# Performance work log

Measured on AMD Instinct MI355X. Metric: run time of the kernel, lower is better.

Reference implementation:

```python
import jax, jax.numpy as jnp
import numpy as np

B, L, P, C = 8, 4, 1024, 256
NH, NS = 8, 4
HD = C // NH  # 32
LEVEL_HW = [(64, 64), (32, 32), (16, 16), (8, 8)]


def setup_inputs() -> dict:
    key = jax.random.key(0)
    ks = jax.random.split(key, 14)
    inp = {
        "x": jax.random.normal(ks[0], (B, L, P, C), jnp.float32),
        # reference points are grid_sample coords in [-1, 1]
        "ref": jax.random.uniform(ks[1], (B, L, P, 2), jnp.float32, -0.9, 0.9),
    }
    for i, (h, w) in enumerate(LEVEL_HW):
        inp[f"feat{i}"] = jax.random.normal(ks[2 + i], (B, C, h, w), jnp.float32)
    inp["w_attn"] = jax.random.normal(ks[6], (C, NH * NS), jnp.float32) * 0.02
    inp["b_attn"] = jax.random.normal(ks[7], (NH * NS,), jnp.float32) * 0.02
    inp["w_off"] = jax.random.normal(ks[8], (C, 2 * NH * NS), jnp.float32) * 0.02
    inp["b_off"] = jax.random.normal(ks[9], (2 * NH * NS,), jnp.float32) * 0.02
    inp["embed_w"] = jax.random.normal(ks[10], (L, C, HD), jnp.float32) * 0.02
    inp["embed_b"] = jax.random.normal(ks[11], (L, HD), jnp.float32) * 0.02
    return inp


def grid_sample_bilinear(feat, grid):
    """torch.F.grid_sample(mode='bilinear', padding_mode='zeros', align_corners=True).
    feat: (B, C, H, W); grid: (B, Gh, Gw, 2) with (x, y) in [-1, 1].
    Returns (B, Gh, Gw, C)  (already permuted vs torch's (B, C, Gh, Gw))."""
    Bn, Cn, H, W = feat.shape
    fx = (grid[..., 0] + 1.0) * 0.5 * (W - 1)  # align_corners=True mapping
    fy = (grid[..., 1] + 1.0) * 0.5 * (H - 1)
    x0f = jnp.floor(fx)
    y0f = jnp.floor(fy)
    x0 = x0f.astype(jnp.int32)
    y0 = y0f.astype(jnp.int32)
    x1 = x0 + 1
    y1 = y0 + 1
    wx1 = fx - x0f
    wy1 = fy - y0f
    wx0 = 1.0 - wx1
    wy0 = 1.0 - wy1
    feat_hwc = jnp.transpose(feat, (0, 2, 3, 1))  # (B, H, W, C)

    def gather(yi, xi):
        valid = ((yi >= 0) & (yi < H) & (xi >= 0) & (xi < W)).astype(feat.dtype)
        yc = jnp.clip(yi, 0, H - 1)
        xc = jnp.clip(xi, 0, W - 1)
        v = jax.vmap(lambda f, y, x: f[y, x])(feat_hwc, yc, xc)  # (B, Gh, Gw, C)
        return v * valid[..., None]

    out = (gather(y0, x0) * (wy0 * wx0)[..., None]
           + gather(y0, x1) * (wy0 * wx1)[..., None]
           + gather(y1, x0) * (wy1 * wx0)[..., None]
           + gather(y1, x1) * (wy1 * wx1)[..., None])
    return out


def reference(x, ref, feat0, feat1, feat2, feat3,
              w_attn, b_attn, w_off, b_off, embed_w, embed_b):
    feats = [feat0, feat1, feat2, feat3]
    b, l, p, c = x.shape
    # attention weights: softmax over samples
    weights = jax.nn.softmax((x @ w_attn + b_attn).reshape(b, l, p, NH, NS), axis=-1)
    # sampling offsets, squashed by tanh
    offsets = jnp.tanh((x @ w_off + b_off).reshape(b, l, p, NH * NS, 2))
    pos = offsets + ref[:, :, :, None, :]  # (b, l, p, NH*NS, 2)
    sampled = []
    for i, f in enumerate(feats):
        s = grid_sample_bilinear(f, pos[:, i])  # (b, p, NH*NS, C_l)
        sampled.append(s @ embed_w[i] + embed_b[i])  # (b, p, NH*NS, HD)
    fs = jnp.stack(sampled, axis=1).reshape(b, l, p, NH, NS, HD)
    out = (weights[..., None] * fs).sum(axis=-2).reshape(b, l, p, NH * HD)
    return out
```

## Files before the change

### kernel.cpp

```cpp
#include <hip/hip_runtime.h>
#include <math.h>

#define B_   8
#define L_   4
#define P_   1024
#define C_   256
#define NH_  8
#define NS_  4
#define HD_  32

typedef _Float16 half8 __attribute__((ext_vector_type(8)));
typedef _Float16 half4 __attribute__((ext_vector_type(4)));
typedef float    f32x4 __attribute__((ext_vector_type(4)));

#define G_F     0u
#define SAMP_F  1392640u
#define WU_F    5586944u
#define ET_F    5611520u

__constant__ const int kGoff[4] = {0, 1048576, 1310720, 1376256};

#define XH2 72
#define LGS 100
#define FTS 40
#define NG_GPROJ 680

__global__ void k0_conv(const float* __restrict__ wa, const float* __restrict__ wo,
                        const float* __restrict__ embed_w,
                        _Float16* __restrict__ WuT, _Float16* __restrict__ ET16) {
  const int bx = blockIdx.x, t = threadIdx.x;
  if (bx < 96) {
    const int n = bx;
    const float v = (n < 32) ? wa[t * 32 + n] : wo[t * 64 + (n - 32)];
    WuT[n * 256 + t] = (_Float16)v;
  } else {
    const int i0 = (bx - 96) * 1024 + t * 4;
    const int l = i0 >> 13, rem = i0 & 8191;
    const int c = rem >> 5, e0 = rem & 31;
    const float4 v = *(const float4*)(embed_w + i0);
    _Float16* d = ET16 + l * 8192 + c;
    d[(e0 + 0) * 256] = (_Float16)v.x;
    d[(e0 + 1) * 256] = (_Float16)v.y;
    d[(e0 + 2) * 256] = (_Float16)v.z;
    d[(e0 + 3) * 256] = (_Float16)v.w;
  }
}

__global__ __launch_bounds__(256) void stage1(
    const float* __restrict__ f0, const float* __restrict__ f1,
    const float* __restrict__ f2, const float* __restrict__ f3,
    const _Float16* __restrict__ ET16, _Float16* __restrict__ g16,
    const float* __restrict__ x,
    const float* __restrict__ ref,
    const _Float16* __restrict__ WuT,
    const float* __restrict__ ba, const float* __restrict__ bo,
    float4* __restrict__ samp4)
{
  __shared__ float4 smraw4[1600];
  const int t = threadIdx.x;
  const int bx = blockIdx.x;
  const int lane = t & 63, wv = t >> 6;
  const int lr = lane & 15, kg = lane >> 4;

  if (bx < NG_GPROJ) {
    _Float16* flT = (_Float16*)smraw4;
    const int b = bx / 85;
    int sub = bx - b * 85, l, tile;
    const float* src;
    if (sub < 64)      { l = 0; tile = sub;      src = f0; }
    else if (sub < 80) { l = 1; tile = sub - 64; src = f1; }
    else if (sub < 84) { l = 2; tile = sub - 80; src = f2; }
    else               { l = 3; tile = 0;        src = f3; }
    const int Wl = 64 >> l, S = Wl * Wl;
    const int s0 = tile * 64;

    const float* sb = src + (size_t)b * C_ * S + s0;
    const _Float16* ETl = ET16 + (size_t)l * 8192;
    const int sl = t & 63, cb = (t >> 6) * 8;

    float vcur[8], vnext[8];
    #pragma unroll
    for (int i = 0; i < 8; ++i) vnext[i] = sb[(size_t)(cb + i) * S + sl];

    f32x4 acc0 = (f32x4){0.f, 0.f, 0.f, 0.f};
    f32x4 acc1 = (f32x4){0.f, 0.f, 0.f, 0.f};

    #pragma unroll
    for (int c = 0; c < 8; ++c) {
      const int c0 = c * 32;
      #pragma unroll
      for (int i = 0; i < 8; ++i) vcur[i] = vnext[i];
      if (c < 7) {
        #pragma unroll
        for (int i = 0; i < 8; ++i)
          vnext[i] = sb[(size_t)(c0 + 32 + cb + i) * S + sl];
      }
      _Float16* fb = flT + (c & 1) * (64 * FTS);
      const half8 hv = {(_Float16)vcur[0], (_Float16)vcur[1], (_Float16)vcur[2], (_Float16)vcur[3],
                        (_Float16)vcur[4], (_Float16)vcur[5], (_Float16)vcur[6], (_Float16)vcur[7]};
      *(half8*)(fb + sl * FTS + cb) = hv;
      __syncthreads();
      const half8 a  = *(const half8*)(fb + (wv * 16 + lr) * FTS + kg * 8);
      const half8 b0 = *(const half8*)(ETl + (size_t)lr * 256 + c0 + kg * 8);
      const half8 b1 = *(const half8*)(ETl + (size_t)(16 + lr) * 256 + c0 + kg * 8);
      acc0 = __builtin_amdgcn_mfma_f32_16x16x32_f16(a, b0, acc0, 0, 0, 0);
      acc1 = __builtin_amdgcn_mfma_f32_16x16x32_f16(a, b1, acc1, 0, 0, 0);
    }

    _Float16* gb = g16 + kGoff[l] + ((size_t)b * S + s0 + wv * 16 + kg * 4) * 32;
    #pragma unroll
    for (int r = 0; r < 4; ++r) {
      gb[r * 32 + lr]      = (_Float16)acc0[r];
      gb[r * 32 + 16 + lr] = (_Float16)acc1[r];
    }
    return;
  }

  _Float16* smx = (_Float16*)smraw4;
  _Float16* smw = (_Float16*)smraw4 + 64 * XH2;
  float*    lg  = (float*)smraw4;

  const int blk = bx - NG_GPROJ;
  const int gp0 = blk * 64;

  f32x4 acc[6];
  #pragma unroll
  for (int nt = 0; nt < 6; ++nt) acc[nt] = (f32x4){0.f, 0.f, 0.f, 0.f};

  #pragma unroll
  for (int chunk = 0; chunk < 4; ++chunk) {
    const int c0 = chunk * 64;
    if (chunk) __syncthreads();
    {
      const int pt = t >> 2, q = t & 3;
      const float4* src = (const float4*)(x + (size_t)(gp0 + pt) * 256 + c0 + q * 16);
      const float4 v0 = src[0], v1 = src[1], v2 = src[2], v3 = src[3];
      _Float16* dst = smx + pt * XH2 + q * 16;
      *(half8*)dst = (half8){(_Float16)v0.x, (_Float16)v0.y, (_Float16)v0.z, (_Float16)v0.w,
                             (_Float16)v1.x, (_Float16)v1.y, (_Float16)v1.z, (_Float16)v1.w};
      *(half8*)(dst + 8) = (half8){(_Float16)v2.x, (_Float16)v2.y, (_Float16)v2.z, (_Float16)v2.w,
                                   (_Float16)v3.x, (_Float16)v3.y, (_Float16)v3.z, (_Float16)v3.w};
    }
    {
      #pragma unroll
      for (int q = 0; q < 3; ++q) {
        const int idx = q * 256 + t;
        const int n = idx >> 3, col8 = idx & 7;
        *(float4*)(smw + n * XH2 + col8 * 8) =
            *(const float4*)(WuT + (size_t)n * 256 + c0 + col8 * 8);
      }
    }
    __syncthreads();

    #pragma unroll
    for (int ks = 0; ks < 2; ++ks) {
      const half8 a = *(const half8*)(smx + (wv * 16 + lr) * XH2 + ks * 32 + kg * 8);
      #pragma unroll
      for (int nt = 0; nt < 6; ++nt) {
        const half8 bf = *(const half8*)(smw + (nt * 16 + lr) * XH2 + ks * 32 + kg * 8);
        acc[nt] = __builtin_amdgcn_mfma_f32_16x16x32_f16(a, bf, acc[nt], 0, 0, 0);
      }
    }
  }
  __syncthreads();

  #pragma unroll
  for (int nt = 0; nt < 6; ++nt) {
    const int n = nt * 16 + lr;
    const float bv = (n < 32) ? ba[n] : bo[n - 32];
    #pragma unroll
    for (int r = 0; r < 4; ++r)
      lg[(wv * 16 + kg * 4 + r) * LGS + n] = acc[nt][r] + bv;
  }
  __syncthreads();

  #pragma unroll
  for (int k = 0; k < 8; ++k) {
    const int slot = k * 256 + t;
    const int pp = slot >> 5, j = slot & 31;
    const int gp = gp0 + pp;
    const int l = (gp >> 10) & 3;
    const int Wl = 64 >> l;
    const float* lgp = lg + pp * LGS;
    const int h4 = (j >> 2) * 4;
    const float l0 = lgp[h4], l1 = lgp[h4 + 1], l2 = lgp[h4 + 2], l3 = lgp[h4 + 3];
    const float m = fmaxf(fmaxf(l0, l1), fmaxf(l2, l3));
    const float e0 = expf(l0 - m), e1 = expf(l1 - m), e2 = expf(l2 - m), e3 = expf(l3 - m);
    const float inv = 1.f / (e0 + e1 + e2 + e3);
    const float es[4] = {e0, e1, e2, e3};
    const float wj = es[j & 3] * inv;
    const float ox = tanhf(lgp[32 + 2 * j])     + ref[(size_t)gp * 2];
    const float oy = tanhf(lgp[32 + 2 * j + 1]) + ref[(size_t)gp * 2 + 1];
    const float sc = 0.5f * (float)(Wl - 1);
    samp4[(size_t)gp * 32 + j] = make_float4(wj, (ox + 1.f) * sc, (oy + 1.f) * sc, 0.f);
  }
}

__global__ __launch_bounds__(256) void k3_main(
    const _Float16* __restrict__ g16,
    const float4* __restrict__ samp4,
    const float* __restrict__ embed_b,
    float* __restrict__ out)
{
  __shared__ int4   tofs[256];
  __shared__ float4 tws[256];
  const int t = threadIdx.x, blk = blockIdx.x;
  const int gp0 = blk * 8;
  const int l = (gp0 >> 10) & 3, b = gp0 >> 12;
  const int Wl = 64 >> l;
  const int gbase = kGoff[l] + b * Wl * Wl * 32;

  {
    const float4 s = samp4[(size_t)gp0 * 32 + t];
    const float fx = s.y, fy = s.z;
    const float x0f = floorf(fx), y0f = floorf(fy);
    const int x0 = (int)x0f, y0 = (int)y0f, x1 = x0 + 1, y1 = y0 + 1;
    const float wx1 = fx - x0f, wy1 = fy - y0f;
    const float wx0 = 1.f - wx1, wy0 = 1.f - wy1;
    const float xv0 = (x0 >= 0 && x0 < Wl) ? 1.f : 0.f;
    const float xv1 = (x1 >= 0 && x1 < Wl) ? 1.f : 0.f;
    const float yv0 = (y0 >= 0 && y0 < Wl) ? 1.f : 0.f;
    const float yv1 = (y1 >= 0 && y1 < Wl) ? 1.f : 0.f;
    const int x0c = min(max(x0, 0), Wl - 1), x1c = min(max(x1, 0), Wl - 1);
    const int y0c = min(max(y0, 0), Wl - 1), y1c = min(max(y1, 0), Wl - 1);
    tofs[t] = make_int4(gbase + (y0c * Wl + x0c) * 32,
                        gbase + (y0c * Wl + x1c) * 32,
                        gbase + (y1c * Wl + x0c) * 32,
                        gbase + (y1c * Wl + x1c) * 32);
    const float w = s.x;
    tws[t] = make_float4(w * wy0 * wx0 * yv0 * xv0,
                         w * wy0 * wx1 * yv0 * xv1,
                         w * wy1 * wx0 * yv1 * xv0,
                         w * wy1 * wx1 * yv1 * xv1);
  }
  __syncthreads();

  const int dq = t & 3, h = (t >> 2) & 7, pt = t >> 5;
  float a[8];
  {
    const float4* bb = (const float4*)(embed_b + l * 32 + dq * 8);
    const float4 b0 = bb[0], b1 = bb[1];
    a[0] = b0.x; a[1] = b0.y; a[2] = b0.z; a[3] = b0.w;
    a[4] = b1.x; a[5] = b1.y; a[6] = b1.z; a[7] = b1.w;
  }
  #pragma unroll
  for (int s = 0; s < 4; ++s) {
    const int slot = pt * 32 + h * 4 + s;
    const int4   o = tofs[slot];
    const float4 w = tws[slot];
    const half8 v00 = *(const half8*)(g16 + o.x + dq * 8);
    const half8 v01 = *(const half8*)(g16 + o.y + dq * 8);
    const half8 v10 = *(const half8*)(g16 + o.z + dq * 8);
    const half8 v11 = *(const half8*)(g16 + o.w + dq * 8);
    #pragma unroll
    for (int j = 0; j < 8; ++j)
      a[j] += w.x * (float)v00[j] + w.y * (float)v01[j]
            + w.z * (float)v10[j] + w.w * (float)v11[j];
  }
  float* od = out + (size_t)(gp0 + pt) * 256 + h * 32 + dq * 8;
  ((float4*)od)[0] = make_float4(a[0], a[1], a[2], a[3]);
  ((float4*)od)[1] = make_float4(a[4], a[5], a[6], a[7]);
}

extern "C" void kernel_launch(void* const* d_in, const int* in_sizes, int n_in,
                              void* d_out, int out_size, void* d_ws, size_t ws_size,
                              hipStream_t stream) {
  const float* x      = (const float*)d_in[0];
  const float* ref    = (const float*)d_in[1];
  const float* w_attn = (const float*)d_in[6];
  const float* b_attn = (const float*)d_in[7];
  const float* w_off  = (const float*)d_in[8];
  const float* b_off  = (const float*)d_in[9];
  const float* emb_w  = (const float*)d_in[10];
  const float* emb_b  = (const float*)d_in[11];
  float* ws  = (float*)d_ws;
  float* out = (float*)d_out;

  _Float16* g16   = (_Float16*)(ws + G_F);
  float4*   samp4 = (float4*)(ws + SAMP_F);
  _Float16* WuT   = (_Float16*)(ws + WU_F);
  _Float16* ET16  = (_Float16*)(ws + ET_F);

  k0_conv<<<128, 256, 0, stream>>>(w_attn, w_off, emb_w, WuT, ET16);

  stage1<<<NG_GPROJ + B_ * L_ * P_ / 64, 256, 0, stream>>>(
      (const float*)d_in[2], (const float*)d_in[3],
      (const float*)d_in[4], (const float*)d_in[5], ET16, g16,
      x, ref, WuT, b_attn, b_off, samp4);

  k3_main<<<B_ * L_ * P_ / 8, 256, 0, stream>>>(g16, samp4, emb_b, out);
}
```

Before: 50.88 us.

## Load MFMA operands directly from global memory, bypassing LDS staging

Both the feature-projection path and the x-projection path now have each lane load its own MFMA A-fragment straight from global memory into registers and convert it to fp16 there. This drops the LDS staging buffers and their per-chunk __syncthreads. Weight B-fragments are also read directly from global memory instead of being copied cooperatively into LDS. The cost is less coalesced, strided global loads (the feature path reads 8 channels at stride S per lane) and more registers, in exchange for fewer barriers and a smaller LDS footprint.

Result: slower. 61.61 us (+21.1%).

```diff
diff --git a/kernel.cpp b/kernel.cpp
--- a/kernel.cpp
+++ b/kernel.cpp
@@ -20,9 +20,7 @@
 
 __constant__ const int kGoff[4] = {0, 1048576, 1310720, 1376256};
 
-#define XH2 72
 #define LGS 100
-#define FTS 40
 #define NG_GPROJ 680
 
 __global__ void k0_conv(const float* __restrict__ wa, const float* __restrict__ wo,
@@ -56,14 +54,13 @@
     const float* __restrict__ ba, const float* __restrict__ bo,
     float4* __restrict__ samp4)
 {
-  __shared__ float4 smraw4[1600];
+  __shared__ float lg[64 * LGS];
   const int t = threadIdx.x;
   const int bx = blockIdx.x;
   const int lane = t & 63, wv = t >> 6;
   const int lr = lane & 15, kg = lane >> 4;
 
   if (bx < NG_GPROJ) {
-    _Float16* flT = (_Float16*)smraw4;
     const int b = bx / 85;
     int sub = bx - b * 85, l, tile;
     const float* src;
@@ -73,34 +70,30 @@
     else               { l = 3; tile = 0;        src = f3; }
     const int Wl = 64 >> l, S = Wl * Wl;
     const int s0 = tile * 64;
-
-    const float* sb = src + (size_t)b * C_ * S + s0;
+    const int srow = s0 + wv * 16 + lr;
+
+    const float* sb = src + (size_t)b * C_ * S + srow;
     const _Float16* ETl = ET16 + (size_t)l * 8192;
-    const int sl = t & 63, cb = (t >> 6) * 8;
-
-    float vcur[8], vnext[8];
-    #pragma unroll
-    for (int i = 0; i < 8; ++i) vnext[i] = sb[(size_t)(cb + i) * S + sl];
 
     f32x4 acc0 = (f32x4){0.f, 0.f, 0.f, 0.f};
     f32x4 acc1 = (f32x4){0.f, 0.f, 0.f, 0.f};
+
+    float vc[8], vn[8];
+    #pragma unroll
+    for (int i = 0; i < 8; ++i) vn[i] = sb[(size_t)(kg * 8 + i) * S];
 
     #pragma unroll
     for (int c = 0; c < 8; ++c) {
       const int c0 = c * 32;
       #pragma unroll
-      for (int i = 0; i < 8; ++i) vcur[i] = vnext[i];
+      for (int i = 0; i < 8; ++i) vc[i] = vn[i];
       if (c < 7) {
         #pragma unroll
         for (int i = 0; i < 8; ++i)
-          vnext[i] = sb[(size_t)(c0 + 32 + cb + i) * S + sl];
+          vn[i] = sb[(size_t)(c0 + 32 + kg * 8 + i) * S];
       }
-      _Float16* fb = flT + (c & 1) * (64 * FTS);
-      const half8 hv = {(_Float16)vcur[0], (_Float16)vcur[1], (_Float16)vcur[2], (_Float16)vcur[3],
-                        (_Float16)vcur[4], (_Float16)vcur[5], (_Float16)vcur[6], (_Float16)vcur[7]};
-      *(half8*)(fb + sl * FTS + cb) = hv;
-      __syncthreads();
-      const half8 a  = *(const half8*)(fb + (wv * 16 + lr) * FTS + kg * 8);
+      const half8 a = {(_Float16)vc[0], (_Float16)vc[1], (_Float16)vc[2], (_Float16)vc[3],
+                       (_Float16)vc[4], (_Float16)vc[5], (_Float16)vc[6], (_Float16)vc[7]};
       const half8 b0 = *(const half8*)(ETl + (size_t)lr * 256 + c0 + kg * 8);
       const half8 b1 = *(const half8*)(ETl + (size_t)(16 + lr) * 256 + c0 + kg * 8);
       acc0 = __builtin_amdgcn_mfma_f32_16x16x32_f16(a, b0, acc0, 0, 0, 0);
@@ -116,53 +109,32 @@
     return;
   }
 
-  _Float16* smx = (_Float16*)smraw4;
-  _Float16* smw = (_Float16*)smraw4 + 64 * XH2;
-  float*    lg  = (float*)smraw4;
-
   const int blk = bx - NG_GPROJ;
   const int gp0 = blk * 64;
 
+  const float* xrow = x + (size_t)(gp0 + wv * 16 + lr) * 256;
+  half8 af[8];
+  #pragma unroll
+  for (int f = 0; f < 8; ++f) {
+    const float4* p = (const float4*)(xrow + f * 32 + kg * 8);
+    const float4 u = p[0], w2 = p[1];
+    af[f] = (half8){(_Float16)u.x,  (_Float16)u.y,  (_Float16)u.z,  (_Float16)u.w,
+                    (_Float16)w2.x, (_Float16)w2.y, (_Float16)w2.z, (_Float16)w2.w};
+  }
+
   f32x4 acc[6];
   #pragma unroll
   for (int nt = 0; nt < 6; ++nt) acc[nt] = (f32x4){0.f, 0.f, 0.f, 0.f};
 
   #pragma unroll
-  for (int chunk = 0; chunk < 4; ++chunk) {
-    const int c0 = chunk * 64;
-    if (chunk) __syncthreads();
-    {
-      const int pt = t >> 2, q = t & 3;
-      const float4* src = (const float4*)(x + (size_t)(gp0 + pt) * 256 + c0 + q * 16);
-      const float4 v0 = src[0], v1 = src[1], v2 = src[2], v3 = src[3];
-      _Float16* dst = smx + pt * XH2 + q * 16;
-      *(half8*)dst = (half8){(_Float16)v0.x, (_Float16)v0.y, (_Float16)v0.z, (_Float16)v0.w,
-                             (_Float16)v1.x, (_Float16)v1.y, (_Float16)v1.z, (_Float16)v1.w};
-      *(half8*)(dst + 8) = (half8){(_Float16)v2.x, (_Float16)v2.y, (_Float16)v2.z, (_Float16)v2.w,
-                                   (_Float16)v3.x, (_Float16)v3.y, (_Float16)v3.z, (_Float16)v3.w};
+  for (int f = 0; f < 8; ++f) {
+    const int koff = f * 32 + kg * 8;
+    #pragma unroll
+    for (int nt = 0; nt < 6; ++nt) {
+      const half8 bf = *(const half8*)(WuT + (size_t)(nt * 16 + lr) * 256 + koff);
+      acc[nt] = __builtin_amdgcn_mfma_f32_16x16x32_f16(af[f], bf, acc[nt], 0, 0, 0);
     }
-    {
-      #pragma unroll
-      for (int q = 0; q < 3; ++q) {
-        const int idx = q * 256 + t;
-        const int n = idx >> 3, col8 = idx & 7;
-        *(float4*)(smw + n * XH2 + col8 * 8) =
-            *(const float4*)(WuT + (size_t)n * 256 + c0 + col8 * 8);
-      }
-    }
-    __syncthreads();
-
-    #pragma unroll
-    for (int ks = 0; ks < 2; ++ks) {
-      const half8 a = *(const half8*)(smx + (wv * 16 + lr) * XH2 + ks * 32 + kg * 8);
-      #pragma unroll
-      for (int nt = 0; nt < 6; ++nt) {
-        const half8 bf = *(const half8*)(smw + (nt * 16 + lr) * XH2 + ks * 32 + kg * 8);
-        acc[nt] = __builtin_amdgcn_mfma_f32_16x16x32_f16(a, bf, acc[nt], 0, 0, 0);
-      }
-    }
-  }
-  __syncthreads();
+  }
 
   #pragma unroll
   for (int nt = 0; nt < 6; ++nt) {
```

## Pre-swizzle projection weights into MFMA fragment order and double-buffer x staging

Applied to the files above, without the earlier changes.

The fp16 projection weights are now written by the conversion kernel in the exact per-lane MFMA B-fragment order, so each lane loads its operand straight from global memory (cache-resident) instead of staging weights through shared memory. The x tile staging now alternates between two shared buffers, which removes one barrier per chunk. This cuts LDS traffic and synchronisation in the projection part of stage1, but adds repeated global loads of the weight fragments in every block, and the second buffer must not overlap the logits region that is used later.

New measurement: 53.00 us. 1.04x slower.

```diff
diff --git a/kernel.cpp b/kernel.cpp
--- a/kernel.cpp
+++ b/kernel.cpp
@@ -10,7 +10,6 @@
 #define HD_  32
 
 typedef _Float16 half8 __attribute__((ext_vector_type(8)));
-typedef _Float16 half4 __attribute__((ext_vector_type(4)));
 typedef float    f32x4 __attribute__((ext_vector_type(4)));
 
 #define G_F     0u
@@ -27,12 +26,14 @@
 
 __global__ void k0_conv(const float* __restrict__ wa, const float* __restrict__ wo,
                         const float* __restrict__ embed_w,
-                        _Float16* __restrict__ WuT, _Float16* __restrict__ ET16) {
+                        _Float16* __restrict__ WuB, _Float16* __restrict__ ET16) {
   const int bx = blockIdx.x, t = threadIdx.x;
   if (bx < 96) {
-    const int n = bx;
-    const float v = (n < 32) ? wa[t * 32 + n] : wo[t * 64 + (n - 32)];
-    WuT[n * 256 + t] = (_Float16)v;
+    const int n = bx, c = t;
+    const float v = (n < 32) ? wa[c * 32 + n] : wo[c * 64 + (n - 32)];
+    const int f = c >> 5, kgw = (c >> 3) & 3, i = c & 7;
+    const int nt = n >> 4, lr = n & 15;
+    WuB[(((f * 6 + nt) * 64) + kgw * 16 + lr) * 8 + i] = (_Float16)v;
   } else {
     const int i0 = (bx - 96) * 1024 + t * 4;
     const int l = i0 >> 13, rem = i0 & 8191;
@@ -52,7 +53,7 @@
     const _Float16* __restrict__ ET16, _Float16* __restrict__ g16,
     const float* __restrict__ x,
     const float* __restrict__ ref,
-    const _Float16* __restrict__ WuT,
+    const _Float16* __restrict__ WuB,
     const float* __restrict__ ba, const float* __restrict__ bo,
     float4* __restrict__ samp4)
 {
@@ -117,7 +118,6 @@
   }
 
   _Float16* smx = (_Float16*)smraw4;
-  _Float16* smw = (_Float16*)smraw4 + 64 * XH2;
   float*    lg  = (float*)smraw4;
 
   const int blk = bx - NG_GPROJ;
@@ -130,34 +130,26 @@
   #pragma unroll
   for (int chunk = 0; chunk < 4; ++chunk) {
     const int c0 = chunk * 64;
-    if (chunk) __syncthreads();
+    _Float16* sx = smx + (chunk & 1) * (64 * XH2);
     {
       const int pt = t >> 2, q = t & 3;
       const float4* src = (const float4*)(x + (size_t)(gp0 + pt) * 256 + c0 + q * 16);
       const float4 v0 = src[0], v1 = src[1], v2 = src[2], v3 = src[3];
-      _Float16* dst = smx + pt * XH2 + q * 16;
+      _Float16* dst = sx + pt * XH2 + q * 16;
       *(half8*)dst = (half8){(_Float16)v0.x, (_Float16)v0.y, (_Float16)v0.z, (_Float16)v0.w,
                              (_Float16)v1.x, (_Float16)v1.y, (_Float16)v1.z, (_Float16)v1.w};
       *(half8*)(dst + 8) = (half8){(_Float16)v2.x, (_Float16)v2.y, (_Float16)v2.z, (_Float16)v2.w,
                                    (_Float16)v3.x, (_Float16)v3.y, (_Float16)v3.z, (_Float16)v3.w};
     }
-    {
-      #pragma unroll
-      for (int q = 0; q < 3; ++q) {
-        const int idx = q * 256 + t;
-        const int n = idx >> 3, col8 = idx & 7;
-        *(float4*)(smw + n * XH2 + col8 * 8) =
-            *(const float4*)(WuT + (size_t)n * 256 + c0 + col8 * 8);
-      }
-    }
     __syncthreads();
 
     #pragma unroll
     for (int ks = 0; ks < 2; ++ks) {
-      const half8 a = *(const half8*)(smx + (wv * 16 + lr) * XH2 + ks * 32 + kg * 8);
+      const int f = chunk * 2 + ks;
+      const half8 a = *(const half8*)(sx + (wv * 16 + lr) * XH2 + ks * 32 + kg * 8);
       #pragma unroll
       for (int nt = 0; nt < 6; ++nt) {
-        const half8 bf = *(const half8*)(smw + (nt * 16 + lr) * XH2 + ks * 32 + kg * 8);
+        const half8 bf = *(const half8*)(WuB + (size_t)((f * 6 + nt) * 64 + lane) * 8);
         acc[nt] = __builtin_amdgcn_mfma_f32_16x16x32_f16(a, bf, acc[nt], 0, 0, 0);
       }
     }
@@ -278,15 +270,15 @@
 
   _Float16* g16   = (_Float16*)(ws + G_F);
   float4*   samp4 = (float4*)(ws + SAMP_F);
-  _Float16* WuT   = (_Float16*)(ws + WU_F);
+  _Float16* WuB   = (_Float16*)(ws + WU_F);
   _Float16* ET16  = (_Float16*)(ws + ET_F);
 
-  k0_conv<<<128, 256, 0, stream>>>(w_attn, w_off, emb_w, WuT, ET16);
+  k0_conv<<<128, 256, 0, stream>>>(w_attn, w_off, emb_w, WuB, ET16);
 
   stage1<<<NG_GPROJ + B_ * L_ * P_ / 64, 256, 0, stream>>>(
       (const float*)d_in[2], (const float*)d_in[3],
       (const float*)d_in[4], (const float*)d_in[5], ET16, g16,
-      x, ref, WuT, b_attn, b_off, samp4);
+      x, ref, WuB, b_attn, b_off, samp4);
 
   k3_main<<<B_ * L_ * P_ / 8, 256, 0, stream>>>(g16, samp4, emb_b, out);
 }
```
